# Performance work log

Hardware: AMD Instinct MI355X
Metric: run time of the kernel (lower is better)

Reference implementation:

```python
import jax, jax.numpy as jnp
import numpy as np
import math

B, S, D, H = 2, 2048, 2048, 16
DH = D // H
SCALE = math.sqrt(DH)


def setup_inputs() -> dict:
    key = jax.random.key(0)
    ks = jax.random.split(key, 9)
    x = jax.random.normal(ks[0], (B, S, D), dtype=jnp.float32)
    # causal mask: True above the diagonal -> masked (matches masked_fill(mask, -inf))
    mask = jnp.triu(jnp.ones((S, S), dtype=jnp.bool_), k=1)
    std = 0.02
    wq = jax.random.normal(ks[1], (D, D), jnp.float32) * std
    wk = jax.random.normal(ks[2], (D, D), jnp.float32) * std
    wv = jax.random.normal(ks[3], (D, D), jnp.float32) * std
    wo = jax.random.normal(ks[4], (D, D), jnp.float32) * std
    bq = jnp.zeros((D,), jnp.float32)
    bk = jnp.zeros((D,), jnp.float32)
    bv = jnp.zeros((D,), jnp.float32)
    bo = jnp.zeros((D,), jnp.float32)
    return {"x": x, "mask": mask, "wq": wq, "bq": bq, "wk": wk, "bk": bk,
            "wv": wv, "bv": bv, "wo": wo, "bo": bo}


def reference(x, mask, wq, bq, wk, bk, wv, bv, wo, bo):
    b, s, d = x.shape
    # projections (nn.Linear: y = x @ W^T + b)
    q = (x @ wq.T + bq).reshape(b, s, H, DH).transpose(0, 2, 1, 3)  # [b,h,s,dh]
    k = (x @ wk.T + bk).reshape(b, s, H, DH).transpose(0, 2, 1, 3)
    v = (x @ wv.T + bv).reshape(b, s, H, DH).transpose(0, 2, 1, 3)
    scores = jnp.einsum('bhqd,bhkd->bhqk', q, k) / SCALE
    scores = jnp.where(mask[None, None, :, :], -jnp.inf, scores)
    attn = jax.nn.softmax(scores, axis=-1)
    out = jnp.einsum('bhqk,bhkd->bhqd', attn, v)  # [b,h,s,dh]
    out = out.transpose(0, 2, 1, 3).reshape(b, s, d)
    return out @ wo.T + bo
```

## Files before the change

kernel.cpp:

```cpp
#include <hip/hip_runtime.h>
#include <hip/hip_bf16.h>


using u16 = unsigned short;
typedef float  f32x4  __attribute__((ext_vector_type(4)));
typedef short  short8 __attribute__((ext_vector_type(8)));

#define DEV __device__ __forceinline__

constexpr int Bc = 2, Sc = 2048, Dc = 2048, Hc = 16, DHc = 128, Mc = 4096, Kc = 2048;
constexpr float RSCALE = 0.08838834764831845f;
constexpr float L2E    = 1.44269504088896341f;

DEV u16 f2bf(float f) { __bf16 h = (__bf16)f; return __builtin_bit_cast(u16, h); }

DEV void gload_lds16(const void* gsrc, void* lds) {
  __builtin_amdgcn_global_load_lds(
      (const __attribute__((address_space(1))) unsigned int*)gsrc,
      (__attribute__((address_space(3))) unsigned int*)lds, 16, 0, 0);
}

__global__ void cast_bf16(const float* __restrict__ in, u16* __restrict__ out, int n4) {
  int i = blockIdx.x * blockDim.x + threadIdx.x;
  if (i >= n4) return;
  float4 v = ((const float4*)in)[i];
  u16 o0 = f2bf(v.x), o1 = f2bf(v.y), o2 = f2bf(v.z), o3 = f2bf(v.w);
  u16* p = out + i * 4;
  p[0] = o0; p[1] = o1; p[2] = o2; p[3] = o3;
}

template <int EPI>
__global__ __launch_bounds__(256) void gemm_bt(
    const u16* __restrict__ A, const u16* __restrict__ W,
    const float* __restrict__ bias0, const float* __restrict__ bias1,
    const float* __restrict__ bias2,
    u16* __restrict__ q_out, u16* __restrict__ k_out, u16* __restrict__ v_out,
    float* __restrict__ f_out) {
  __shared__ u16 lsA[2][128 * 32];
  __shared__ u16 lsB[2][128 * 32];
  const int tid = threadIdx.x;
  const int lane = tid & 63;
  const int w = tid >> 6;
  const int wr = w >> 1, wc = w & 1;
  const int l15 = lane & 15, l4 = lane >> 4;
  const int m0 = blockIdx.y * 128;
  const int n0 = blockIdx.x * 128;

  f32x4 acc[4][4] = {};

  auto stage = [&](int buf, int t) {
    const int k0 = t * 32;
#pragma unroll
    for (int c = 0; c < 2; ++c) {
      int p = c * 256 + tid;
      int row = p >> 2;
      int lg = (p & 3) ^ (row & 3);
      gload_lds16(A + (size_t)(m0 + row) * Kc + k0 + lg * 8, &lsA[buf][p * 8]);
    }
#pragma unroll
    for (int c = 0; c < 2; ++c) {
      int p = c * 256 + tid;
      int row = p >> 2;
      int lg = (p & 3) ^ (row & 3);
      gload_lds16(W + (size_t)(n0 + row) * Kc + k0 + lg * 8, &lsB[buf][p * 8]);
    }
  };

  auto compute = [&](int buf) {
    short8 af[4], bf[4];
#pragma unroll
    for (int mf = 0; mf < 4; ++mf) {
      int row = wr * 64 + mf * 16 + l15;
      int pc = l4 ^ (row & 3);
      af[mf] = *(const short8*)&lsA[buf][row * 32 + pc * 8];
    }
#pragma unroll
    for (int nf = 0; nf < 4; ++nf) {
      int row = wc * 64 + nf * 16 + l15;
      int pc = l4 ^ (row & 3);
      bf[nf] = *(const short8*)&lsB[buf][row * 32 + pc * 8];
    }
#pragma unroll
    for (int mf = 0; mf < 4; ++mf)
#pragma unroll
      for (int nf = 0; nf < 4; ++nf)
        acc[mf][nf] = __builtin_amdgcn_mfma_f32_16x16x32_bf16(af[mf], bf[nf], acc[mf][nf], 0, 0, 0);
  };

  stage(0, 0);
  __syncthreads();
  int buf = 0;
  const int NT = Kc / 32;
  for (int t = 0; t < NT - 1; ++t) {
    stage(buf ^ 1, t + 1);
    compute(buf);
    __syncthreads();
    buf ^= 1;
  }
  compute(buf);

  if constexpr (EPI == 0) {
#pragma unroll
    for (int nf = 0; nf < 4; ++nf) {
      const int n = n0 + wc * 64 + nf * 16 + l15;
      const int sec = n >> 11;
      const int n2 = n & 2047;
      const float bias = sec == 0 ? bias0[n2] : (sec == 1 ? bias1[n2] : bias2[n2]);
      const float scl = sec == 0 ? RSCALE : 1.0f;
      u16* dst = sec == 0 ? q_out : (sec == 1 ? k_out : v_out);
      const int h = n2 >> 7, dh = n2 & 127;
#pragma unroll
      for (int mf = 0; mf < 4; ++mf)
#pragma unroll
        for (int r = 0; r < 4; ++r) {
          const int m = m0 + wr * 64 + mf * 16 + l4 * 4 + r;
          const int bb = m >> 11, s = m & 2047;
          dst[((size_t)(bb * Hc + h) * Sc + s) * DHc + dh] = f2bf((acc[mf][nf][r] + bias) * scl);
        }
    }
  } else {
#pragma unroll
    for (int nf = 0; nf < 4; ++nf) {
      const int n = n0 + wc * 64 + nf * 16 + l15;
      const float bias = bias0[n];
#pragma unroll
      for (int mf = 0; mf < 4; ++mf)
#pragma unroll
        for (int r = 0; r < 4; ++r) {
          const int m = m0 + wr * 64 + mf * 16 + l4 * 4 + r;
          f_out[(size_t)m * Dc + n] = acc[mf][nf][r] + bias;
        }
    }
  }
}

__global__ void transpose_v(const u16* __restrict__ V, u16* __restrict__ VT) {
  __shared__ u16 t[32][33];
  const int bh = blockIdx.z;
  const int s0 = blockIdx.x * 32;
  const int d0 = blockIdx.y * 32;
  const int tx = threadIdx.x, ty = threadIdx.y;
#pragma unroll
  for (int k = 0; k < 4; ++k)
    t[ty + 8 * k][tx] = V[((size_t)bh * Sc + s0 + ty + 8 * k) * DHc + d0 + tx];
  __syncthreads();
#pragma unroll
  for (int k = 0; k < 4; ++k)
    VT[((size_t)bh * DHc + d0 + ty + 8 * k) * Sc + s0 + tx] = t[tx][ty + 8 * k];
}

__global__ __launch_bounds__(256) void fattn(
    const u16* __restrict__ Qb, const u16* __restrict__ Kb,
    const u16* __restrict__ VTb, u16* __restrict__ AO) {
  __shared__ u16 lsK[2][64 * 128];
  __shared__ u16 lsV[2][128 * 64];
  __shared__ u16 lsP[4][16 * 64];

  const int tid = threadIdx.x;
  const int lane = tid & 63;
  const int w = tid >> 6;
  const int l15 = lane & 15, l4 = lane >> 4;

  const int id = blockIdx.x;
  const int xcd = id & 7, seq = id >> 3;
  const int bh = xcd + 8 * (seq >> 4);
  const int pair = seq & 15;

  const int b = bh >> 4, h = bh & 15;
  const size_t kbase = (size_t)bh * Sc * DHc;
  const size_t vbase = (size_t)bh * DHc * Sc;

#pragma unroll 1
  for (int qsel = 0; qsel < 2; ++qsel) {
    const int qt = qsel ? (31 - pair) : pair;
    const int q0 = qt * 64;
    const int ntiles = qt + 1;

    const size_t qbase = ((size_t)bh * Sc + q0 + w * 16 + l15) * DHc;
    short8 qf[4];
#pragma unroll
    for (int ks = 0; ks < 4; ++ks)
      qf[ks] = *(const short8*)&Qb[qbase + ks * 32 + l4 * 8];

    float m_run[4], l_run[4];
#pragma unroll
    for (int r = 0; r < 4; ++r) { m_run[r] = -__builtin_inff(); l_run[r] = 0.f; }
    f32x4 o_acc[8] = {};

    auto stageKV = [&](int sb, int ti) {
      const int kv0 = ti * 64;
#pragma unroll
      for (int c = 0; c < 4; ++c) {
        int p = c * 256 + tid;
        int row = p >> 4, ph = p & 15;
        int lg = (ph & 8) | ((ph ^ row) & 7);
        gload_lds16(Kb + kbase + (size_t)(kv0 + row) * DHc + lg * 8, &lsK[sb][p * 8]);
      }
#pragma unroll
      for (int c = 0; c < 4; ++c) {
        int p = c * 256 + tid;
        int row = p >> 3, ph = p & 7;
        int lg = ph ^ (row & 7);
        gload_lds16(VTb + vbase + (size_t)row * Sc + kv0 + lg * 8, &lsV[sb][p * 8]);
      }
    };

    stageKV(0, 0);
    asm volatile("s_waitcnt vmcnt(0)" ::: "memory");
    __syncthreads();

    int buf = 0;
#pragma unroll 1
    for (int ti = 0; ti < ntiles; ++ti) {
      const int kv0 = ti * 64;
      if (ti + 1 < ntiles) stageKV(buf ^ 1, ti + 1);

      f32x4 s[4] = {};
      __builtin_amdgcn_s_setprio(1);
#pragma unroll
      for (int nf = 0; nf < 4; ++nf) {
        int row = nf * 16 + l15;
#pragma unroll
        for (int ks = 0; ks < 4; ++ks) {
          int lg = ks * 4 + l4;
          int pc = (lg & 8) | ((lg ^ row) & 7);
          short8 kf = *(const short8*)&lsK[buf][row * 128 + pc * 8];
          s[nf] = __builtin_amdgcn_mfma_f32_16x16x32_bf16(qf[ks], kf, s[nf], 0, 0, 0);
        }
      }
      __builtin_amdgcn_s_setprio(0);

      if (kv0 == q0) {
#pragma unroll
        for (int nf = 0; nf < 4; ++nf) {
          int kc = nf * 16 + l15;
#pragma unroll
          for (int r = 0; r < 4; ++r)
            if (kc > w * 16 + l4 * 4 + r) s[nf][r] = -__builtin_inff();
        }
      }
      float alpha[4];
#pragma unroll
      for (int r = 0; r < 4; ++r) {
        float mx = fmaxf(fmaxf(s[0][r], s[1][r]), fmaxf(s[2][r], s[3][r]));
        mx = fmaxf(mx, __shfl_xor(mx, 1));
        mx = fmaxf(mx, __shfl_xor(mx, 2));
        mx = fmaxf(mx, __shfl_xor(mx, 4));
        mx = fmaxf(mx, __shfl_xor(mx, 8));
        float mnew = fmaxf(m_run[r], mx);
        alpha[r] = __builtin_amdgcn_exp2f((m_run[r] - mnew) * L2E);
        m_run[r] = mnew;
      }
#pragma unroll
      for (int nf = 0; nf < 4; ++nf)
#pragma unroll
        for (int r = 0; r < 4; ++r)
          s[nf][r] = __builtin_amdgcn_exp2f((s[nf][r] - m_run[r]) * L2E);
#pragma unroll
      for (int r = 0; r < 4; ++r) {
        float sm = s[0][r] + s[1][r] + s[2][r] + s[3][r];
        sm += __shfl_xor(sm, 1);
        sm += __shfl_xor(sm, 2);
        sm += __shfl_xor(sm, 4);
        sm += __shfl_xor(sm, 8);
        l_run[r] = l_run[r] * alpha[r] + sm;
      }
#pragma unroll
      for (int nf2 = 0; nf2 < 8; ++nf2)
#pragma unroll
        for (int r = 0; r < 4; ++r) o_acc[nf2][r] *= alpha[r];

#pragma unroll
      for (int nf = 0; nf < 4; ++nf)
#pragma unroll
        for (int r = 0; r < 4; ++r) {
          int rif = l4 * 4 + r;
          int kc = nf * 16 + l15;
          int pc = (kc >> 3) ^ (rif & 7);
          lsP[w][rif * 64 + pc * 8 + (kc & 7)] = f2bf(s[nf][r]);
        }
      asm volatile("s_waitcnt lgkmcnt(0)" ::: "memory");

      __builtin_amdgcn_s_setprio(1);
#pragma unroll
      for (int ks = 0; ks < 2; ++ks) {
        int pc = (ks * 4 + l4) ^ (l15 & 7);
        short8 pa = *(const short8*)&lsP[w][l15 * 64 + pc * 8];
#pragma unroll
        for (int nf2 = 0; nf2 < 8; ++nf2) {
          int vrow = nf2 * 16 + l15;
          int vpc = (ks * 4 + l4) ^ (vrow & 7);
          short8 vb = *(const short8*)&lsV[buf][vrow * 64 + vpc * 8];
          o_acc[nf2] = __builtin_amdgcn_mfma_f32_16x16x32_bf16(pa, vb, o_acc[nf2], 0, 0, 0);
        }
      }
      __builtin_amdgcn_s_setprio(0);

      asm volatile("s_waitcnt vmcnt(0)" ::: "memory");
      __syncthreads();
      buf ^= 1;
    }

#pragma unroll
    for (int nf2 = 0; nf2 < 8; ++nf2)
#pragma unroll
      for (int r = 0; r < 4; ++r) {
        int qr = q0 + w * 16 + l4 * 4 + r;
        float ov = o_acc[nf2][r] / l_run[r];
        AO[((size_t)(b * Sc + qr)) * Dc + h * DHc + nf2 * 16 + l15] = f2bf(ov);
      }
    __syncthreads();
  }
}

extern "C" void kernel_launch(void* const* d_in, const int* in_sizes, int n_in,
                              void* d_out, int out_size, void* d_ws, size_t ws_size,
                              hipStream_t stream) {
  const float* x  = (const float*)d_in[0];
  const float* wq = (const float*)d_in[2];
  const float* bq = (const float*)d_in[3];
  const float* wk = (const float*)d_in[4];
  const float* bk = (const float*)d_in[5];
  const float* wv = (const float*)d_in[6];
  const float* bv = (const float*)d_in[7];
  const float* wo = (const float*)d_in[8];
  const float* bo = (const float*)d_in[9];
  float* out = (float*)d_out;

  char* ws = (char*)d_ws;
  u16* WQKV = (u16*)(ws + 0);
  u16* WOb  = (u16*)(ws + 25165824);
  u16* XB   = (u16*)(ws + 33554432);
  u16* Qb   = (u16*)(ws + 50331648);
  u16* Kb   = (u16*)(ws + 67108864);
  u16* Vb   = (u16*)(ws + 83886080);
  u16* VTb  = (u16*)(ws + 100663296);
  u16* AO   = XB;

  cast_bf16<<<dim3(8192), dim3(256), 0, stream>>>(x, XB, Mc * Dc / 4);
  cast_bf16<<<dim3(4096), dim3(256), 0, stream>>>(wq, WQKV, Dc * Dc / 4);
  cast_bf16<<<dim3(4096), dim3(256), 0, stream>>>(wk, WQKV + (size_t)Dc * Dc, Dc * Dc / 4);
  cast_bf16<<<dim3(4096), dim3(256), 0, stream>>>(wv, WQKV + (size_t)2 * Dc * Dc, Dc * Dc / 4);
  cast_bf16<<<dim3(4096), dim3(256), 0, stream>>>(wo, WOb, Dc * Dc / 4);

  gemm_bt<0><<<dim3(48, 32), dim3(256), 0, stream>>>(XB, WQKV, bq, bk, bv, Qb, Kb, Vb, nullptr);
  transpose_v<<<dim3(64, 4, 32), dim3(32, 8), 0, stream>>>(Vb, VTb);
  fattn<<<dim3(512), dim3(256), 0, stream>>>(Qb, Kb, VTb, AO);
  gemm_bt<1><<<dim3(16, 32), dim3(256), 0, stream>>>(AO, WOb, bo, nullptr, nullptr,
                                                     nullptr, nullptr, nullptr, out);
}
```

Baseline: 440.6 us.

## Replace QKV projection with 256x256 8-wave pipelined GEMM and fuse casts

The QKV projection moves to a new kernel with 512 threads and 256x256 output tiles over a 64-wide K step. It uses XOR-swizzled LDS, direct global-to-LDS loads, a quarter-split schedule that interleaves loads with MFMA phases, s_setprio, and a block-ID remap for L2 locality. The five separate fp32-to-bf16 cast launches are merged into one kernel. The aim is more data reuse per tile and better overlap of memory and MFMA work in the largest GEMM, at the cost of high register and LDS pressure (128 KB LDS per block) and a hand-tuned waitcnt schedule that is fragile.

```diff
diff --git a/kernel.cpp b/kernel.cpp
--- a/kernel.cpp
+++ b/kernel.cpp
@@ -20,22 +20,154 @@
       (__attribute__((address_space(3))) unsigned int*)lds, 16, 0, 0);
 }
 
-__global__ void cast_bf16(const float* __restrict__ in, u16* __restrict__ out, int n4) {
-  int i = blockIdx.x * blockDim.x + threadIdx.x;
-  if (i >= n4) return;
-  float4 v = ((const float4*)in)[i];
+__global__ void cast_all(const float* __restrict__ x, const float* __restrict__ wq,
+                         const float* __restrict__ wk, const float* __restrict__ wv,
+                         const float* __restrict__ wo, u16* __restrict__ XB,
+                         u16* __restrict__ WQKV, u16* __restrict__ WOb) {
+  const int i = blockIdx.x * blockDim.x + threadIdx.x;
+  const float4* src;
+  u16* dst;
+  if (i < 2097152)      { src = (const float4*)x  + i;             dst = XB   + (size_t)i * 4; }
+  else if (i < 3145728) { src = (const float4*)wq + (i - 2097152); dst = WQKV + (size_t)(i - 2097152) * 4; }
+  else if (i < 4194304) { src = (const float4*)wk + (i - 3145728); dst = WQKV + 4194304 + (size_t)(i - 3145728) * 4; }
+  else if (i < 5242880) { src = (const float4*)wv + (i - 4194304); dst = WQKV + 8388608 + (size_t)(i - 4194304) * 4; }
+  else                  { src = (const float4*)wo + (i - 5242880); dst = WOb  + (size_t)(i - 5242880) * 4; }
+  float4 v = *src;
   u16 o0 = f2bf(v.x), o1 = f2bf(v.y), o2 = f2bf(v.z), o3 = f2bf(v.w);
-  u16* p = out + i * 4;
-  p[0] = o0; p[1] = o1; p[2] = o2; p[3] = o3;
-}
-
-template <int EPI>
-__global__ __launch_bounds__(256) void gemm_bt(
+  dst[0] = o0; dst[1] = o1; dst[2] = o2; dst[3] = o3;
+}
+
+__global__ __launch_bounds__(512, 2) void gemm8p_qkv(
     const u16* __restrict__ A, const u16* __restrict__ W,
-    const float* __restrict__ bias0, const float* __restrict__ bias1,
-    const float* __restrict__ bias2,
-    u16* __restrict__ q_out, u16* __restrict__ k_out, u16* __restrict__ v_out,
-    float* __restrict__ f_out) {
+    const float* __restrict__ bq, const float* __restrict__ bk,
+    const float* __restrict__ bv,
+    u16* __restrict__ q_out, u16* __restrict__ k_out, u16* __restrict__ v_out) {
+  __shared__ u16 lsA[2][256 * 64];
+  __shared__ u16 lsB[2][256 * 64];
+  const int tid = threadIdx.x;
+  const int lane = tid & 63;
+  const int w = tid >> 6;
+  const int wr = w >> 2, wc = w & 3;
+  const int l15 = lane & 15, l4 = lane >> 4;
+
+  const int id = blockIdx.x;
+  const int wg = (id & 7) * 48 + (id >> 3);
+  const int bx = wg >> 4;
+  const int by = wg & 15;
+  const int m0 = by * 256, n0 = bx * 256;
+
+  constexpr int NT = Kc / 64;
+
+  const int srow = tid >> 3;
+  const int spc = tid & 7;
+  const int slc = spc ^ (srow & 7);
+
+  auto stA = [&](int buf, int t, int mq, int h) {
+    const int r = h * 128 + mq * 64 + srow;
+    gload_lds16(A + (size_t)(m0 + r) * Kc + t * 64 + slc * 8,
+                &lsA[buf][(h * 128 + mq * 64) * 64 + tid * 8]);
+  };
+  auto stB = [&](int buf, int t, int nq, int j) {
+    const int rr = j * 64 + srow;
+    const int n = nq * 32 + (rr >> 5) * 64 + (rr & 31);
+    gload_lds16(W + (size_t)(n0 + n) * Kc + t * 64 + slc * 8,
+                &lsB[buf][(nq * 128 + j * 64) * 64 + tid * 8]);
+  };
+
+  const int pc0 = l4 ^ (l15 & 7);
+  const int pc1 = (4 + l4) ^ (l15 & 7);
+  const int rA = wr * 128 + l15;
+  const int rB = wc * 32 + l15;
+
+  f32x4 acc[8][4] = {};
+  short8 af[8], b0[4], b1[4];
+
+  auto ldA = [&](int buf, int mq) {
+#pragma unroll
+    for (int fm = 0; fm < 4; ++fm) {
+      const u16* base = &lsA[buf][(rA + mq * 64 + fm * 16) * 64];
+      af[fm * 2 + 0] = *(const short8*)(base + pc0 * 8);
+      af[fm * 2 + 1] = *(const short8*)(base + pc1 * 8);
+    }
+  };
+  auto ldB = [&](int buf, int nq, short8* bf) {
+#pragma unroll
+    for (int fr = 0; fr < 2; ++fr) {
+      const u16* base = &lsB[buf][(nq * 128 + rB + fr * 16) * 64];
+      bf[fr * 2 + 0] = *(const short8*)(base + pc0 * 8);
+      bf[fr * 2 + 1] = *(const short8*)(base + pc1 * 8);
+    }
+  };
+  auto mma = [&](const short8* bf, int mo, int no) {
+#pragma unroll
+    for (int ks = 0; ks < 2; ++ks)
+#pragma unroll
+      for (int fm = 0; fm < 4; ++fm)
+#pragma unroll
+        for (int fr = 0; fr < 2; ++fr)
+          acc[mo + fm][no + fr] = __builtin_amdgcn_mfma_f32_16x16x32_bf16(
+              af[fm * 2 + ks], bf[fr * 2 + ks], acc[mo + fm][no + fr], 0, 0, 0);
+  };
+
+  stA(0, 0, 0, 0); stA(0, 0, 0, 1); stA(0, 0, 1, 0); stA(0, 0, 1, 1);
+  stB(0, 0, 0, 0); stB(0, 0, 0, 1); stB(0, 0, 1, 0); stB(0, 0, 1, 1);
+  stA(1, 1, 0, 0); stA(1, 1, 0, 1); stB(1, 1, 0, 0); stB(1, 1, 0, 1);
+  asm volatile("s_waitcnt vmcnt(4)" ::: "memory");
+  __builtin_amdgcn_s_barrier();
+
+#pragma unroll 1
+  for (int u = 0; u < NT; ++u) {
+    const int c = u & 1;
+    ldA(c, 0); ldB(c, 0, b0);
+    if (u + 1 < NT) { stA(c ^ 1, u + 1, 1, 0); stA(c ^ 1, u + 1, 1, 1); }
+    __builtin_amdgcn_s_barrier();
+    asm volatile("s_waitcnt lgkmcnt(0)" ::: "memory");
+    __builtin_amdgcn_s_setprio(1); mma(b0, 0, 0); __builtin_amdgcn_s_setprio(0);
+    __builtin_amdgcn_s_barrier();
+    ldB(c, 1, b1);
+    if (u + 1 < NT) { stB(c ^ 1, u + 1, 1, 0); stB(c ^ 1, u + 1, 1, 1); }
+    __builtin_amdgcn_s_barrier();
+    asm volatile("s_waitcnt lgkmcnt(0)" ::: "memory");
+    __builtin_amdgcn_s_setprio(1); mma(b1, 0, 2); __builtin_amdgcn_s_setprio(0);
+    __builtin_amdgcn_s_barrier();
+    ldA(c, 1);
+    if (u + 2 < NT) { stA(c, u + 2, 0, 0); stA(c, u + 2, 0, 1); }
+    __builtin_amdgcn_s_barrier();
+    asm volatile("s_waitcnt lgkmcnt(0)" ::: "memory");
+    __builtin_amdgcn_s_setprio(1); mma(b0, 4, 0); __builtin_amdgcn_s_setprio(0);
+    __builtin_amdgcn_s_barrier();
+    if (u + 2 < NT) { stB(c, u + 2, 0, 0); stB(c, u + 2, 0, 1); }
+    __builtin_amdgcn_s_barrier();
+    __builtin_amdgcn_s_setprio(1); mma(b1, 4, 2); __builtin_amdgcn_s_setprio(0);
+    if (u + 2 < NT)      asm volatile("s_waitcnt vmcnt(4)" ::: "memory");
+    else if (u + 1 < NT) asm volatile("s_waitcnt vmcnt(0)" ::: "memory");
+    __builtin_amdgcn_s_barrier();
+  }
+
+  const int sec = n0 >> 11;
+  const int n0s = n0 & 2047;
+  const float* bias = sec == 0 ? bq : (sec == 1 ? bk : bv);
+  u16* dst = sec == 0 ? q_out : (sec == 1 ? k_out : v_out);
+  const float scl = sec == 0 ? RSCALE : 1.0f;
+#pragma unroll
+  for (int fg = 0; fg < 4; ++fg) {
+    const int n2 = n0s + wc * 64 + fg * 16 + l15;
+    const float bv_ = bias[n2];
+    const int h = n2 >> 7, dh = n2 & 127;
+#pragma unroll
+    for (int fmg = 0; fmg < 8; ++fmg)
+#pragma unroll
+      for (int r = 0; r < 4; ++r) {
+        const int m = m0 + wr * 128 + fmg * 16 + l4 * 4 + r;
+        const int bb = m >> 11, s = m & 2047;
+        dst[((size_t)(bb * Hc + h) * Sc + s) * DHc + dh] = f2bf((acc[fmg][fg][r] + bv_) * scl);
+      }
+  }
+}
+
+__global__ __launch_bounds__(256) void gemm_bt_out(
+    const u16* __restrict__ A, const u16* __restrict__ W,
+    const float* __restrict__ bias0, float* __restrict__ f_out) {
   __shared__ u16 lsA[2][128 * 32];
   __shared__ u16 lsB[2][128 * 32];
   const int tid = threadIdx.x;
@@ -99,38 +231,17 @@
   }
   compute(buf);
 
-  if constexpr (EPI == 0) {
-#pragma unroll
-    for (int nf = 0; nf < 4; ++nf) {
-      const int n = n0 + wc * 64 + nf * 16 + l15;
-      const int sec = n >> 11;
-      const int n2 = n & 2047;
-      const float bias = sec == 0 ? bias0[n2] : (sec == 1 ? bias1[n2] : bias2[n2]);
-      const float scl = sec == 0 ? RSCALE : 1.0f;
-      u16* dst = sec == 0 ? q_out : (sec == 1 ? k_out : v_out);
-      const int h = n2 >> 7, dh = n2 & 127;
-#pragma unroll
-      for (int mf = 0; mf < 4; ++mf)
-#pragma unroll
-        for (int r = 0; r < 4; ++r) {
-          const int m = m0 + wr * 64 + mf * 16 + l4 * 4 + r;
-          const int bb = m >> 11, s = m & 2047;
-          dst[((size_t)(bb * Hc + h) * Sc + s) * DHc + dh] = f2bf((acc[mf][nf][r] + bias) * scl);
-        }
-    }
-  } else {
-#pragma unroll
-    for (int nf = 0; nf < 4; ++nf) {
-      const int n = n0 + wc * 64 + nf * 16 + l15;
-      const float bias = bias0[n];
-#pragma unroll
-      for (int mf = 0; mf < 4; ++mf)
-#pragma unroll
-        for (int r = 0; r < 4; ++r) {
-          const int m = m0 + wr * 64 + mf * 16 + l4 * 4 + r;
-          f_out[(size_t)m * Dc + n] = acc[mf][nf][r] + bias;
-        }
-    }
+#pragma unroll
+  for (int nf = 0; nf < 4; ++nf) {
+    const int n = n0 + wc * 64 + nf * 16 + l15;
+    const float bias = bias0[n];
+#pragma unroll
+    for (int mf = 0; mf < 4; ++mf)
+#pragma unroll
+      for (int r = 0; r < 4; ++r) {
+        const int m = m0 + wr * 64 + mf * 16 + l4 * 4 + r;
+        f_out[(size_t)m * Dc + n] = acc[mf][nf][r] + bias;
+      }
   }
 }
 
@@ -337,15 +448,9 @@
   u16* VTb  = (u16*)(ws + 100663296);
   u16* AO   = XB;
 
-  cast_bf16<<<dim3(8192), dim3(256), 0, stream>>>(x, XB, Mc * Dc / 4);
-  cast_bf16<<<dim3(4096), dim3(256), 0, stream>>>(wq, WQKV, Dc * Dc / 4);
-  cast_bf16<<<dim3(4096), dim3(256), 0, stream>>>(wk, WQKV + (size_t)Dc * Dc, Dc * Dc / 4);
-  cast_bf16<<<dim3(4096), dim3(256), 0, stream>>>(wv, WQKV + (size_t)2 * Dc * Dc, Dc * Dc / 4);
-  cast_bf16<<<dim3(4096), dim3(256), 0, stream>>>(wo, WOb, Dc * Dc / 4);
-
-  gemm_bt<0><<<dim3(48, 32), dim3(256), 0, stream>>>(XB, WQKV, bq, bk, bv, Qb, Kb, Vb, nullptr);
+  cast_all<<<dim3(24576), dim3(256), 0, stream>>>(x, wq, wk, wv, wo, XB, WQKV, WOb);
+  gemm8p_qkv<<<dim3(384), dim3(512), 0, stream>>>(XB, WQKV, bq, bk, bv, Qb, Kb, Vb);
   transpose_v<<<dim3(64, 4, 32), dim3(32, 8), 0, stream>>>(Vb, VTb);
   fattn<<<dim3(512), dim3(256), 0, stream>>>(Qb, Kb, VTb, AO);
-  gemm_bt<1><<<dim3(16, 32), dim3(256), 0, stream>>>(AO, WOb, bo, nullptr, nullptr,
-                                                     nullptr, nullptr, nullptr, out);
-}
+  gemm_bt_out<<<dim3(16, 32), dim3(256), 0, stream>>>(AO, WOb, bo, out);
+}
```

Result: no change. 445.7 us (+1.2%).
